# Optimization experiments

Measured on AMD Instinct MI355X. Metric: run time of the kernel, lower is better.

## Reference

```python
import jax, jax.numpy as jnp
import numpy as np

N_HEAD = 8
HID = 64
IN_DIM = 512
OUT_DIM = 512


def setup_inputs() -> dict:
    key = jax.random.key(0)
    ks = jax.random.split(key, 12)
    B, LQ, LK = 2, 2048, 2048
    stdv = 1.0 / np.sqrt(HID)
    inp = {
        "q": jax.random.normal(ks[0], (B, LQ, IN_DIM), jnp.float32),
        "k": jax.random.normal(ks[1], (B, LK, IN_DIM), jnp.float32),
        "v": jax.random.normal(ks[2], (B, LK, IN_DIM), jnp.float32),
        # linear params stored as (in, out); torch Linear applies x @ W.T + b,
        # we store pre-transposed weights so y = x @ W + b is the same math.
        "Wq": jax.random.normal(ks[3], (IN_DIM, N_HEAD * HID), jnp.float32) * 0.02,
        "bq": jnp.zeros((N_HEAD * HID,), jnp.float32),
        "Wk": jax.random.normal(ks[4], (IN_DIM, N_HEAD * HID), jnp.float32) * 0.02,
        "bk": jnp.zeros((N_HEAD * HID,), jnp.float32),
        "Wv": jax.random.normal(ks[5], (IN_DIM, N_HEAD * HID), jnp.float32) * 0.02,
        "bv": jnp.zeros((N_HEAD * HID,), jnp.float32),
        # mlp-method scoring vector, uniform(-stdv, stdv), length 2*hidden
        "w_score": jax.random.uniform(ks[6], (2 * HID,), jnp.float32, -stdv, stdv),
        "Wd": jax.random.normal(ks[7], (N_HEAD * HID, OUT_DIM), jnp.float32) * 0.02,
        "bd": jnp.zeros((OUT_DIM,), jnp.float32),
    }
    return inp


def reference(q, k, v, Wq, bq, Wk, bk, Wv, bv, w_score, Wd, bd):
    B, Lq, _ = q.shape
    Lk = k.shape[1]
    # project and split heads -> (n_head, B, L, hid), matching torch's
    # permute(2,0,1,3).view(n_head*B, L, hid) layout
    qx = (q @ Wq + bq).reshape(B, Lq, N_HEAD, HID).transpose(2, 0, 1, 3)
    kx = (k @ Wk + bk).reshape(B, Lk, N_HEAD, HID).transpose(2, 0, 1, 3)
    vx = (v @ Wv + bv).reshape(B, Lk, N_HEAD, HID).transpose(2, 0, 1, 3)
    # 'mlp' additive attention: tanh(cat(q_i, k_j) . w) == tanh(q_i.w1 + k_j.w2)
    # computed as a broadcast sum instead of materializing the concat tensor
    w1, w2 = w_score[:HID], w_score[HID:]
    qw = qx @ w1  # (n_head, B, Lq)
    kw = kx @ w2  # (n_head, B, Lk)
    score = jnp.tanh(qw[..., :, None] + kw[..., None, :])  # (n_head, B, Lq, Lk)
    score = jax.nn.softmax(score, axis=-1)
    out_head = jnp.einsum('hbqk,hbkd->hbqd', score, vx)  # (n_head, B, Lq, hid)
    # torch: split along head*batch dim then cat along features -> head-major concat
    out = out_head.transpose(1, 2, 0, 3).reshape(B, Lq, N_HEAD * HID)
    output = out @ Wd + bd  # dropout is identity in eval
    score_flat = score.reshape(N_HEAD * B, Lq, Lk)
    return output, score_flat
```

## Files before the change

kernel.cpp:

```cpp
#include <hip/hip_runtime.h>
#include <math.h>

#define B_  2
#define L_  2048
#define D_  512
#define NH_ 8
#define HD_ 64

typedef __attribute__((ext_vector_type(8))) short short8;
typedef __attribute__((ext_vector_type(4))) float f32x4;

__device__ __forceinline__ float ex2(float x) {
#if __has_builtin(__builtin_amdgcn_exp2f)
    return __builtin_amdgcn_exp2f(x);
#else
    return exp2f(x);
#endif
}
__device__ __forceinline__ float rcp_(float x) {
#if __has_builtin(__builtin_amdgcn_rcpf)
    return __builtin_amdgcn_rcpf(x);
#else
    return 1.0f / x;
#endif
}

__device__ __forceinline__ float fast_e(float x) {
    float z  = ex2(x * 2.885390082f);
    float th = 1.0f - 2.0f * rcp_(z + 1.0f);
    return ex2(th * 1.4426950408889634f);
}

__device__ __forceinline__ unsigned int f2bf(float x) {
    unsigned int u = __float_as_uint(x);
    u += 0x7fffu + ((u >> 16) & 1u);
    return u >> 16;
}
__device__ __forceinline__ unsigned int pk2(float lo, float hi) {
    return f2bf(lo) | (f2bf(hi) << 16);
}

__global__ void k_prep(const float* __restrict__ Wq, const float* __restrict__ bq,
                       const float* __restrict__ Wk, const float* __restrict__ bk,
                       const float* __restrict__ wsc,
                       float* __restrict__ wqwT, float* __restrict__ wkwT,
                       float* __restrict__ bqw, float* __restrict__ bkw) {
    __shared__ float w[HD_];
    int which = blockIdx.x >> 1;
    int half  = blockIdx.x & 1;
    const float* W  = which ? Wk : Wq;
    const float* bb = which ? bk : bq;
    float* WT = which ? wkwT : wqwT;
    float* bo = which ? bkw  : bqw;
    if (threadIdx.x < HD_) w[threadIdx.x] = wsc[which * HD_ + threadIdx.x];
    __syncthreads();
    int r = half * 256 + threadIdx.x;
    for (int h = 0; h < NH_; ++h) {
        float s = 0.f;
        #pragma unroll 8
        for (int d = 0; d < HD_; ++d) s += W[r * D_ + h * HD_ + d] * w[d];
        WT[h * D_ + r] = s;
    }
    if (half == 0 && threadIdx.x < NH_) {
        int h = threadIdx.x;
        float s = 0.f;
        for (int d = 0; d < HD_; ++d) s += bb[h * HD_ + d] * w[d];
        bo[h] = s;
    }
}

__global__ void k_wconv(const float* __restrict__ Wv, const float* __restrict__ Wd,
                        unsigned short* __restrict__ WvF,
                        unsigned short* __restrict__ WdFh,
                        unsigned short* __restrict__ WdFl) {
    int id = blockIdx.x * 256 + threadIdx.x;
    int lane = id & 63;
    int kb = (id >> 6) & 15;
    int nf = id >> 10;
    int l15 = lane & 15, lg = lane >> 4;
    int n = nf * 16 + l15;
    int k0 = kb * 32 + lg * 4;
    size_t base = ((size_t)(nf * 16 + kb) * 64 + lane) * 8;
    if (blockIdx.y == 0) {
        #pragma unroll
        for (int j = 0; j < 8; ++j) {
            int k = k0 + (j & 3) + 16 * (j >> 2);
            WvF[base + j] = (unsigned short)f2bf(Wv[(size_t)k * 512 + n]);
        }
    } else {
        #pragma unroll
        for (int j = 0; j < 8; ++j) {
            int k = k0 + (j & 3) + 16 * (j >> 2);
            float x = Wd[(size_t)k * 512 + n];
            unsigned int h = f2bf(x);
            float hf = __uint_as_float(h << 16);
            WdFh[base + j] = (unsigned short)h;
            WdFl[base + j] = (unsigned short)f2bf(x - hf);
        }
    }
}

__global__ void k_qwkw(const float* __restrict__ q, const float* __restrict__ k,
                       const float* __restrict__ wqwT, const float* __restrict__ wkwT,
                       const float* __restrict__ bqw, const float* __restrict__ bkw,
                       float* __restrict__ qw, float* __restrict__ kw) {
    int wid  = blockIdx.x * 4 + (threadIdx.x >> 6);
    int lane = threadIdx.x & 63;
    int sel  = wid >= 4096;
    int row  = wid & 4095;
    const float* src = sel ? k : q;
    const float* WT  = sel ? wkwT : wqwT;
    const float* bo  = sel ? bkw : bqw;
    float* dst = sel ? kw : qw;
    float4 va = *(const float4*)(src + (size_t)row * D_ + lane * 4);
    float4 vb = *(const float4*)(src + (size_t)row * D_ + 256 + lane * 4);
    float res[NH_];
    #pragma unroll
    for (int h = 0; h < NH_; ++h) {
        float4 wa = *(const float4*)(WT + h * D_ + lane * 4);
        float4 wb = *(const float4*)(WT + h * D_ + 256 + lane * 4);
        float s = va.x*wa.x + va.y*wa.y + va.z*wa.z + va.w*wa.w
                + vb.x*wb.x + vb.y*wb.y + vb.z*wb.z + vb.w*wb.w;
        #pragma unroll
        for (int off = 32; off; off >>= 1) s += __shfl_xor(s, off);
        res[h] = s + bo[h];
    }
    if (lane == 0) {
        #pragma unroll
        for (int h = 0; h < NH_; ++h) dst[h * 4096 + row] = res[h];
    }
}

__global__ __launch_bounds__(256) void k_rsum(const float* __restrict__ qw,
                                              const float* __restrict__ kw,
                                              float* __restrict__ rsum) {
    int hb   = blockIdx.y;
    int widx = threadIdx.x >> 6;
    int lane = threadIdx.x & 63;
    int r = blockIdx.x * 4 + widx;
    float qwv = qw[hb * 2048 + r];
    const float* kp = kw + hb * 2048;
    float s = 0.f;
    #pragma unroll
    for (int j = 0; j < 8; ++j) {
        float4 v = *(const float4*)(kp + j * 256 + lane * 4);
        s += (fast_e(qwv + v.x) + fast_e(qwv + v.y))
           + (fast_e(qwv + v.z) + fast_e(qwv + v.w));
    }
    #pragma unroll
    for (int off = 32; off; off >>= 1) s += __shfl_xor(s, off);
    if (lane == 0) rsum[hb * 2048 + r] = 1.0f / s;
}

__global__ __launch_bounds__(256) void k_mmA(const float* __restrict__ A,
                                             const short8* __restrict__ BF,
                                             const float* __restrict__ bias,
                                             unsigned short* __restrict__ vxg) {
    int m0 = blockIdx.x * 64;
    int n0q = blockIdx.y * 4;
    int tid = threadIdx.x;
    int w = tid >> 6, lane = tid & 63;
    int l15 = lane & 15, lg = lane >> 4;
    f32x4 acc[4];
    #pragma unroll
    for (int j = 0; j < 4; ++j) acc[j] = (f32x4){0.f, 0.f, 0.f, 0.f};

    const float* a0 = A + (size_t)(m0 + w * 16 + l15) * 512 + lg * 4;

    float4 clo = *(const float4*)(a0);
    float4 chi = *(const float4*)(a0 + 16);
    short8 cb[4];
    #pragma unroll
    for (int nf = 0; nf < 4; ++nf) cb[nf] = BF[(size_t)(n0q + nf) * 16 * 64 + lane];

    for (int kb = 0; kb < 16; ++kb) {
        float4 lo = clo, hi = chi;
        short8 b0 = cb[0], b1 = cb[1], b2 = cb[2], b3 = cb[3];
        if (kb < 15) {
            clo = *(const float4*)(a0 + (kb + 1) * 32);
            chi = *(const float4*)(a0 + (kb + 1) * 32 + 16);
            #pragma unroll
            for (int nf = 0; nf < 4; ++nf)
                cb[nf] = BF[((size_t)(n0q + nf) * 16 + kb + 1) * 64 + lane];
        }
        union { unsigned int u[4]; short8 s; } af;
        af.u[0] = pk2(lo.x, lo.y); af.u[1] = pk2(lo.z, lo.w);
        af.u[2] = pk2(hi.x, hi.y); af.u[3] = pk2(hi.z, hi.w);
        acc[0] = __builtin_amdgcn_mfma_f32_16x16x32_bf16(af.s, b0, acc[0], 0, 0, 0);
        acc[1] = __builtin_amdgcn_mfma_f32_16x16x32_bf16(af.s, b1, acc[1], 0, 0, 0);
        acc[2] = __builtin_amdgcn_mfma_f32_16x16x32_bf16(af.s, b2, acc[2], 0, 0, 0);
        acc[3] = __builtin_amdgcn_mfma_f32_16x16x32_bf16(af.s, b3, acc[3], 0, 0, 0);
    }
    #pragma unroll
    for (int nf = 0; nf < 4; ++nf) {
        int n = (n0q + nf) * 16 + l15;
        float bvv = bias[n];
        int h = n >> 6, dt = (n >> 4) & 3, ncol = n & 15;
        #pragma unroll
        for (int r = 0; r < 4; ++r) {
            int m = m0 + w * 16 + lg * 4 + r;
            int b = m >> 11, kk = m & 2047;
            int kblk = kk >> 5, k32 = kk & 31;
            int lane_v = ncol + 16 * ((k32 >> 2) & 3);
            int ie = (k32 & 3) + 4 * (k32 >> 4);
            size_t ad = ((((size_t)(h * 2 + b) * 64 + kblk) * 4 + dt) * 64 + lane_v) * 8 + ie;
            vxg[ad] = (unsigned short)f2bf(acc[nf][r] + bvv);
        }
    }
}

__global__ __launch_bounds__(256) void k_mmB(const float* __restrict__ A,
                                             const short8* __restrict__ BFh,
                                             const short8* __restrict__ BFl,
                                             const float* __restrict__ bias,
                                             float* __restrict__ C) {
    int m0 = blockIdx.x * 64;
    int n0q = blockIdx.y * 4;
    int tid = threadIdx.x;
    int w = tid >> 6, lane = tid & 63;
    int l15 = lane & 15, lg = lane >> 4;
    f32x4 acc[4];
    #pragma unroll
    for (int j = 0; j < 4; ++j) acc[j] = (f32x4){0.f, 0.f, 0.f, 0.f};

    const float* a0 = A + (size_t)(m0 + w * 16 + l15) * 512 + lg * 4;

    float4 clo = *(const float4*)(a0);
    float4 chi = *(const float4*)(a0 + 16);

    for (int kb = 0; kb < 16; ++kb) {
        float4 lo = clo, hi = chi;
        if (kb < 15) {
            clo = *(const float4*)(a0 + (kb + 1) * 32);
            chi = *(const float4*)(a0 + (kb + 1) * 32 + 16);
        }
        union { unsigned int u[4]; short8 s; } ah, al;
        {
            float xs[8] = {lo.x, lo.y, lo.z, lo.w, hi.x, hi.y, hi.z, hi.w};
            unsigned int hu[8]; float lf[8];
            #pragma unroll
            for (int j = 0; j < 8; ++j) {
                hu[j] = f2bf(xs[j]);
                lf[j] = xs[j] - __uint_as_float(hu[j] << 16);
            }
            #pragma unroll
            for (int j = 0; j < 4; ++j) {
                ah.u[j] = hu[2 * j] | (hu[2 * j + 1] << 16);
                al.u[j] = pk2(lf[2 * j], lf[2 * j + 1]);
            }
        }
        #pragma unroll
        for (int nf = 0; nf < 4; ++nf) {
            size_t bi = ((size_t)(n0q + nf) * 16 + kb) * 64 + lane;
            short8 bh = BFh[bi];
            short8 bl = BFl[bi];
            acc[nf] = __builtin_amdgcn_mfma_f32_16x16x32_bf16(ah.s, bh, acc[nf], 0, 0, 0);
            acc[nf] = __builtin_amdgcn_mfma_f32_16x16x32_bf16(al.s, bh, acc[nf], 0, 0, 0);
            acc[nf] = __builtin_amdgcn_mfma_f32_16x16x32_bf16(ah.s, bl, acc[nf], 0, 0, 0);
        }
    }
    #pragma unroll
    for (int nf = 0; nf < 4; ++nf) {
        int n = (n0q + nf) * 16 + l15;
        float bdv = bias[n];
        #pragma unroll
        for (int r = 0; r < 4; ++r) {
            int m = m0 + w * 16 + lg * 4 + r;
            C[(size_t)m * 512 + n] = acc[nf][r] + bdv;
        }
    }
}

__global__ __launch_bounds__(512, 4) void k_main(const float* __restrict__ qw,
                                                 const float* __restrict__ kw,
                                                 const short8* __restrict__ vgs,
                                                 const float* __restrict__ rsum,
                                                 float* __restrict__ att,
                                                 float* __restrict__ score) {
    int hb  = blockIdx.y;
    int q0  = blockIdx.x * 64;
    int tid = threadIdx.x;
    int w   = tid >> 6;
    int wq  = w & 3;
    int kh  = w >> 2;
    int lane = tid & 63;
    int l15 = lane & 15, lg = lane >> 4;

    __shared__ float kws[2048];
    __shared__ float red[4][16][68];

    *(float4*)&kws[tid * 4] = *(const float4*)(kw + hb * 2048 + tid * 4);
    __syncthreads();

    int qrow = q0 + wq * 16 + l15;
    float qwv = qw[hb * 2048 + qrow];
    float rs  = rsum[hb * 2048 + qrow];
    const short8* bp = vgs + (size_t)hb * 16384 + lane;

    f32x4 acc0 = {0,0,0,0}, acc1 = {0,0,0,0}, acc2 = {0,0,0,0}, acc3 = {0,0,0,0};

    int kb0 = kh * 32;
    const short8* pb = bp + (size_t)kb0 * 256;
    short8 cb0 = pb[0], cb1 = pb[64], cb2 = pb[128], cb3 = pb[192];
    float4 ckw0 = *(const float4*)&kws[kb0 * 32 + lg * 4];
    float4 ckw1 = *(const float4*)&kws[kb0 * 32 + lg * 4 + 16];

    float* sp = score + ((size_t)(hb * 2048 + qrow)) * 2048 + kb0 * 32 + lg * 4;

    for (int i = 0; i < 32; ++i) {
        short8 b0 = cb0, b1 = cb1, b2 = cb2, b3 = cb3;
        float4 kw0 = ckw0, kw1 = ckw1;
        if (i < 31) {
            const short8* nb = bp + (size_t)(kb0 + i + 1) * 256;
            cb0 = nb[0]; cb1 = nb[64]; cb2 = nb[128]; cb3 = nb[192];
            int nk = (kb0 + i + 1) * 32 + lg * 4;
            ckw0 = *(const float4*)&kws[nk];
            ckw1 = *(const float4*)&kws[nk + 16];
        }
        float e0 = fast_e(qwv + kw0.x) * rs, e1 = fast_e(qwv + kw0.y) * rs;
        float e2 = fast_e(qwv + kw0.z) * rs, e3 = fast_e(qwv + kw0.w) * rs;
        float e4 = fast_e(qwv + kw1.x) * rs, e5 = fast_e(qwv + kw1.y) * rs;
        float e6 = fast_e(qwv + kw1.z) * rs, e7 = fast_e(qwv + kw1.w) * rs;
        union { unsigned int u[4]; short8 s; } af;
        af.u[0] = pk2(e0, e1);
        af.u[1] = pk2(e2, e3);
        af.u[2] = pk2(e4, e5);
        af.u[3] = pk2(e6, e7);
        acc0 = __builtin_amdgcn_mfma_f32_16x16x32_bf16(af.s, b0, acc0, 0, 0, 0);
        acc1 = __builtin_amdgcn_mfma_f32_16x16x32_bf16(af.s, b1, acc1, 0, 0, 0);
        acc2 = __builtin_amdgcn_mfma_f32_16x16x32_bf16(af.s, b2, acc2, 0, 0, 0);
        acc3 = __builtin_amdgcn_mfma_f32_16x16x32_bf16(af.s, b3, acc3, 0, 0, 0);
        float4 s0 = {e0, e1, e2, e3};
        float4 s1 = {e4, e5, e6, e7};
        *(float4*)(sp + i * 32)      = s0;
        *(float4*)(sp + i * 32 + 16) = s1;
    }

    if (kh == 1) {
        #define WR_(dt, accv) \
            red[wq][lg * 4 + 0][dt * 16 + l15] = accv[0]; \
            red[wq][lg * 4 + 1][dt * 16 + l15] = accv[1]; \
            red[wq][lg * 4 + 2][dt * 16 + l15] = accv[2]; \
            red[wq][lg * 4 + 3][dt * 16 + l15] = accv[3];
        WR_(0, acc0) WR_(1, acc1) WR_(2, acc2) WR_(3, acc3)
        #undef WR_
    }
    __syncthreads();
    if (kh == 0) {
        int b_ = hb & 1, h = hb >> 1;
        float* ab = att + ((size_t)(b_ * 2048 + q0 + wq * 16 + lg * 4)) * 512 + h * 64 + l15;
        #define ST_(dt, accv) \
            ab[0 * 512 + dt * 16] = accv[0] + red[wq][lg * 4 + 0][dt * 16 + l15]; \
            ab[1 * 512 + dt * 16] = accv[1] + red[wq][lg * 4 + 1][dt * 16 + l15]; \
            ab[2 * 512 + dt * 16] = accv[2] + red[wq][lg * 4 + 2][dt * 16 + l15]; \
            ab[3 * 512 + dt * 16] = accv[3] + red[wq][lg * 4 + 3][dt * 16 + l15];
        ST_(0, acc0) ST_(1, acc1) ST_(2, acc2) ST_(3, acc3)
        #undef ST_
    }
}

extern "C" void kernel_launch(void* const* d_in, const int* in_sizes, int n_in,
                              void* d_out, int out_size, void* d_ws, size_t ws_size,
                              hipStream_t stream) {
    (void)in_sizes; (void)n_in; (void)out_size; (void)ws_size;
    const float* q   = (const float*)d_in[0];
    const float* k   = (const float*)d_in[1];
    const float* v   = (const float*)d_in[2];
    const float* Wq  = (const float*)d_in[3];
    const float* bq  = (const float*)d_in[4];
    const float* Wk  = (const float*)d_in[5];
    const float* bk  = (const float*)d_in[6];
    const float* Wv  = (const float*)d_in[7];
    const float* bv  = (const float*)d_in[8];
    const float* wsc = (const float*)d_in[9];
    const float* Wd  = (const float*)d_in[10];
    const float* bd  = (const float*)d_in[11];

    float* out   = (float*)d_out;
    float* score = out + (size_t)B_ * L_ * D_;

    float* ws    = (float*)d_ws;
    float* wqwT  = ws;
    float* wkwT  = ws + 4096;
    float* bqw   = ws + 8192;
    float* bkw   = ws + 8256;
    float* qw    = ws + 8704;
    float* kw    = ws + 41472;
    float* rsum  = ws + 74240;
    float* vxg   = ws + 107008;
    float* att   = ws + 1155584;
    float* WvF   = ws + 3252736;
    float* WdFh  = ws + 3383808;
    float* WdFl  = ws + 3514880;

    k_prep<<<dim3(4), dim3(256), 0, stream>>>(Wq, bq, Wk, bk, wsc, wqwT, wkwT, bqw, bkw);
    k_wconv<<<dim3(128, 2), dim3(256), 0, stream>>>(Wv, Wd,
        (unsigned short*)WvF, (unsigned short*)WdFh, (unsigned short*)WdFl);
    k_qwkw<<<dim3(2048), dim3(256), 0, stream>>>(q, k, wqwT, wkwT, bqw, bkw, qw, kw);
    k_rsum<<<dim3(512, 16), dim3(256), 0, stream>>>(qw, kw, rsum);
    k_mmA<<<dim3(64, 8), dim3(256), 0, stream>>>(v, (const short8*)WvF, bv,
        (unsigned short*)vxg);
    k_main<<<dim3(32, 16), dim3(512), 0, stream>>>(qw, kw, (const short8*)vxg,
        rsum, att, score);
    k_mmB<<<dim3(64, 8), dim3(256), 0, stream>>>(att, (const short8*)WdFh,
        (const short8*)WdFl, bd, out);
}
```

Baseline: 165.5 us.

## Split score writing and PV matmul into interleaved specialized blocks in one launch

The main attention kernel is replaced by a fused launch of 2560 blocks. Every fifth block computes the P·V MFMA accumulation and writes att but no longer stores score. The other blocks each write 16 full score rows with coalesced float4 stores, recomputing the exponentials. This separates the memory-bound score store (about 268 MB) from the MFMA work so that the two kinds of blocks can overlap on the GPU, at the cost of computing the exp values twice.

```diff
diff --git a/kernel.cpp b/kernel.cpp
--- a/kernel.cpp
+++ b/kernel.cpp
@@ -271,91 +271,112 @@
     }
 }
 
-__global__ __launch_bounds__(512, 4) void k_main(const float* __restrict__ qw,
-                                                 const float* __restrict__ kw,
-                                                 const short8* __restrict__ vgs,
-                                                 const float* __restrict__ rsum,
-                                                 float* __restrict__ att,
-                                                 float* __restrict__ score) {
-    int hb  = blockIdx.y;
-    int q0  = blockIdx.x * 64;
+__global__ __launch_bounds__(512, 4) void k_fused(const float* __restrict__ qw,
+                                                  const float* __restrict__ kw,
+                                                  const short8* __restrict__ vgs,
+                                                  const float* __restrict__ rsum,
+                                                  float* __restrict__ att,
+                                                  float* __restrict__ score) {
+    __shared__ float smem[2048 + 4 * 16 * 68];
+    float* kws = smem;
+    int bx  = blockIdx.x;
     int tid = threadIdx.x;
-    int w   = tid >> 6;
-    int wq  = w & 3;
-    int kh  = w >> 2;
-    int lane = tid & 63;
-    int l15 = lane & 15, lg = lane >> 4;
-
-    __shared__ float kws[2048];
-    __shared__ float red[4][16][68];
-
-    *(float4*)&kws[tid * 4] = *(const float4*)(kw + hb * 2048 + tid * 4);
-    __syncthreads();
-
-    int qrow = q0 + wq * 16 + l15;
-    float qwv = qw[hb * 2048 + qrow];
-    float rs  = rsum[hb * 2048 + qrow];
-    const short8* bp = vgs + (size_t)hb * 16384 + lane;
-
-    f32x4 acc0 = {0,0,0,0}, acc1 = {0,0,0,0}, acc2 = {0,0,0,0}, acc3 = {0,0,0,0};
-
-    int kb0 = kh * 32;
-    const short8* pb = bp + (size_t)kb0 * 256;
-    short8 cb0 = pb[0], cb1 = pb[64], cb2 = pb[128], cb3 = pb[192];
-    float4 ckw0 = *(const float4*)&kws[kb0 * 32 + lg * 4];
-    float4 ckw1 = *(const float4*)&kws[kb0 * 32 + lg * 4 + 16];
-
-    float* sp = score + ((size_t)(hb * 2048 + qrow)) * 2048 + kb0 * 32 + lg * 4;
-
-    for (int i = 0; i < 32; ++i) {
-        short8 b0 = cb0, b1 = cb1, b2 = cb2, b3 = cb3;
-        float4 kw0 = ckw0, kw1 = ckw1;
-        if (i < 31) {
-            const short8* nb = bp + (size_t)(kb0 + i + 1) * 256;
-            cb0 = nb[0]; cb1 = nb[64]; cb2 = nb[128]; cb3 = nb[192];
-            int nk = (kb0 + i + 1) * 32 + lg * 4;
-            ckw0 = *(const float4*)&kws[nk];
-            ckw1 = *(const float4*)&kws[nk + 16];
-        }
-        float e0 = fast_e(qwv + kw0.x) * rs, e1 = fast_e(qwv + kw0.y) * rs;
-        float e2 = fast_e(qwv + kw0.z) * rs, e3 = fast_e(qwv + kw0.w) * rs;
-        float e4 = fast_e(qwv + kw1.x) * rs, e5 = fast_e(qwv + kw1.y) * rs;
-        float e6 = fast_e(qwv + kw1.z) * rs, e7 = fast_e(qwv + kw1.w) * rs;
-        union { unsigned int u[4]; short8 s; } af;
-        af.u[0] = pk2(e0, e1);
-        af.u[1] = pk2(e2, e3);
-        af.u[2] = pk2(e4, e5);
-        af.u[3] = pk2(e6, e7);
-        acc0 = __builtin_amdgcn_mfma_f32_16x16x32_bf16(af.s, b0, acc0, 0, 0, 0);
-        acc1 = __builtin_amdgcn_mfma_f32_16x16x32_bf16(af.s, b1, acc1, 0, 0, 0);
-        acc2 = __builtin_amdgcn_mfma_f32_16x16x32_bf16(af.s, b2, acc2, 0, 0, 0);
-        acc3 = __builtin_amdgcn_mfma_f32_16x16x32_bf16(af.s, b3, acc3, 0, 0, 0);
-        float4 s0 = {e0, e1, e2, e3};
-        float4 s1 = {e4, e5, e6, e7};
-        *(float4*)(sp + i * 32)      = s0;
-        *(float4*)(sp + i * 32 + 16) = s1;
-    }
-
-    if (kh == 1) {
-        #define WR_(dt, accv) \
-            red[wq][lg * 4 + 0][dt * 16 + l15] = accv[0]; \
-            red[wq][lg * 4 + 1][dt * 16 + l15] = accv[1]; \
-            red[wq][lg * 4 + 2][dt * 16 + l15] = accv[2]; \
-            red[wq][lg * 4 + 3][dt * 16 + l15] = accv[3];
-        WR_(0, acc0) WR_(1, acc1) WR_(2, acc2) WR_(3, acc3)
-        #undef WR_
-    }
-    __syncthreads();
-    if (kh == 0) {
-        int b_ = hb & 1, h = hb >> 1;
-        float* ab = att + ((size_t)(b_ * 2048 + q0 + wq * 16 + lg * 4)) * 512 + h * 64 + l15;
-        #define ST_(dt, accv) \
-            ab[0 * 512 + dt * 16] = accv[0] + red[wq][lg * 4 + 0][dt * 16 + l15]; \
-            ab[1 * 512 + dt * 16] = accv[1] + red[wq][lg * 4 + 1][dt * 16 + l15]; \
-            ab[2 * 512 + dt * 16] = accv[2] + red[wq][lg * 4 + 2][dt * 16 + l15]; \
-            ab[3 * 512 + dt * 16] = accv[3] + red[wq][lg * 4 + 3][dt * 16 + l15];
-        ST_(0, acc0) ST_(1, acc1) ST_(2, acc2) ST_(3, acc3)
-        #undef ST_
+
+    if (bx % 5 == 0) {
+        int mb = bx / 5;
+        int hb = mb >> 5;
+        int q0 = (mb & 31) * 64;
+        int w   = tid >> 6;
+        int wq  = w & 3;
+        int kh  = w >> 2;
+        int lane = tid & 63;
+        int l15 = lane & 15, lg = lane >> 4;
+        float (*red)[68] = (float(*)[68])(smem + 2048);
+
+        *(float4*)&kws[tid * 4] = *(const float4*)(kw + hb * 2048 + tid * 4);
+        __syncthreads();
+
+        int qrow = q0 + wq * 16 + l15;
+        float qwv = qw[hb * 2048 + qrow];
+        float rs  = rsum[hb * 2048 + qrow];
+        const short8* bp = vgs + (size_t)hb * 16384 + lane;
+
+        f32x4 acc0 = {0,0,0,0}, acc1 = {0,0,0,0}, acc2 = {0,0,0,0}, acc3 = {0,0,0,0};
+
+        int kb0 = kh * 32;
+        const short8* pb = bp + (size_t)kb0 * 256;
+        short8 cb0 = pb[0], cb1 = pb[64], cb2 = pb[128], cb3 = pb[192];
+        float4 ckw0 = *(const float4*)&kws[kb0 * 32 + lg * 4];
+        float4 ckw1 = *(const float4*)&kws[kb0 * 32 + lg * 4 + 16];
+
+        for (int i = 0; i < 32; ++i) {
+            short8 b0 = cb0, b1 = cb1, b2 = cb2, b3 = cb3;
+            float4 kw0 = ckw0, kw1 = ckw1;
+            if (i < 31) {
+                const short8* nb = bp + (size_t)(kb0 + i + 1) * 256;
+                cb0 = nb[0]; cb1 = nb[64]; cb2 = nb[128]; cb3 = nb[192];
+                int nk = (kb0 + i + 1) * 32 + lg * 4;
+                ckw0 = *(const float4*)&kws[nk];
+                ckw1 = *(const float4*)&kws[nk + 16];
+            }
+            float e0 = fast_e(qwv + kw0.x) * rs, e1 = fast_e(qwv + kw0.y) * rs;
+            float e2 = fast_e(qwv + kw0.z) * rs, e3 = fast_e(qwv + kw0.w) * rs;
+            float e4 = fast_e(qwv + kw1.x) * rs, e5 = fast_e(qwv + kw1.y) * rs;
+            float e6 = fast_e(qwv + kw1.z) * rs, e7 = fast_e(qwv + kw1.w) * rs;
+            union { unsigned int u[4]; short8 s; } af;
+            af.u[0] = pk2(e0, e1);
+            af.u[1] = pk2(e2, e3);
+            af.u[2] = pk2(e4, e5);
+            af.u[3] = pk2(e6, e7);
+            acc0 = __builtin_amdgcn_mfma_f32_16x16x32_bf16(af.s, b0, acc0, 0, 0, 0);
+            acc1 = __builtin_amdgcn_mfma_f32_16x16x32_bf16(af.s, b1, acc1, 0, 0, 0);
+            acc2 = __builtin_amdgcn_mfma_f32_16x16x32_bf16(af.s, b2, acc2, 0, 0, 0);
+            acc3 = __builtin_amdgcn_mfma_f32_16x16x32_bf16(af.s, b3, acc3, 0, 0, 0);
+        }
+
+        if (kh == 1) {
+            #define WR_(dt, accv) \
+                red[wq * 16 + lg * 4 + 0][dt * 16 + l15] = accv[0]; \
+                red[wq * 16 + lg * 4 + 1][dt * 16 + l15] = accv[1]; \
+                red[wq * 16 + lg * 4 + 2][dt * 16 + l15] = accv[2]; \
+                red[wq * 16 + lg * 4 + 3][dt * 16 + l15] = accv[3];
+            WR_(0, acc0) WR_(1, acc1) WR_(2, acc2) WR_(3, acc3)
+            #undef WR_
+        }
+        __syncthreads();
+        if (kh == 0) {
+            int b_ = hb & 1, h = hb >> 1;
+            float* ab = att + ((size_t)(b_ * 2048 + q0 + wq * 16 + lg * 4)) * 512 + h * 64 + l15;
+            #define ST_(dt, accv) \
+                ab[0 * 512 + dt * 16] = accv[0] + red[wq * 16 + lg * 4 + 0][dt * 16 + l15]; \
+                ab[1 * 512 + dt * 16] = accv[1] + red[wq * 16 + lg * 4 + 1][dt * 16 + l15]; \
+                ab[2 * 512 + dt * 16] = accv[2] + red[wq * 16 + lg * 4 + 2][dt * 16 + l15]; \
+                ab[3 * 512 + dt * 16] = accv[3] + red[wq * 16 + lg * 4 + 3][dt * 16 + l15];
+            ST_(0, acc0) ST_(1, acc1) ST_(2, acc2) ST_(3, acc3)
+            #undef ST_
+        }
+    } else {
+        int sb = bx - bx / 5 - 1;
+        int hb = sb >> 7;
+        int q0 = (sb & 127) * 16;
+        *(float4*)&kws[tid * 4] = *(const float4*)(kw + hb * 2048 + tid * 4);
+        __syncthreads();
+        int rl  = tid >> 5;
+        int t32 = tid & 31;
+        int q = q0 + rl;
+        float qwv = qw[hb * 2048 + q];
+        float rsq = rsum[hb * 2048 + q];
+        float* outp = score + ((size_t)(hb * 2048 + q)) * 2048;
+        #pragma unroll
+        for (int i = 0; i < 16; ++i) {
+            int k = i * 128 + t32 * 4;
+            float4 o;
+            o.x = fast_e(qwv + kws[k + 0]) * rsq;
+            o.y = fast_e(qwv + kws[k + 1]) * rsq;
+            o.z = fast_e(qwv + kws[k + 2]) * rsq;
+            o.w = fast_e(qwv + kws[k + 3]) * rsq;
+            *(float4*)(outp + k) = o;
+        }
     }
 }
 
@@ -400,7 +421,7 @@
     k_rsum<<<dim3(512, 16), dim3(256), 0, stream>>>(qw, kw, rsum);
     k_mmA<<<dim3(64, 8), dim3(256), 0, stream>>>(v, (const short8*)WvF, bv,
         (unsigned short*)vxg);
-    k_main<<<dim3(32, 16), dim3(512), 0, stream>>>(qw, kw, (const short8*)vxg,
+    k_fused<<<dim3(2560), dim3(512), 0, stream>>>(qw, kw, (const short8*)vxg,
         rsum, att, score);
     k_mmB<<<dim3(64, 8), dim3(256), 0, stream>>>(att, (const short8*)WdFh,
         (const short8*)WdFl, bd, out);
```

Measured after the change: 196.1 us. 1.18x slower.
